# Kernel optimization log

Hardware: AMD Instinct MI355X
Metric: run time of the kernel (lower is better)

The kernel has to match this reference:

```python
import jax, jax.numpy as jnp
import numpy as np

B, S, HID, NH = 2, 2048, 1024, 16
HD = HID // NH  # head_dim = 64


def setup_inputs() -> dict:
    key = jax.random.key(0)
    ks = jax.random.split(key, 11)
    sc = 1.0 / np.sqrt(HID)
    inp = {
        "query": jax.random.normal(ks[0], (B, S, HID), jnp.float32),
        "key_": jax.random.normal(ks[1], (B, S, HID), jnp.float32),
        "value": jax.random.normal(ks[2], (B, S, HID), jnp.float32),
        "Wq": jax.random.normal(ks[3], (HID, HID), jnp.float32) * sc,
        "bq": jnp.zeros((HID,), jnp.float32),
        "Wk": jax.random.normal(ks[4], (HID, HID), jnp.float32) * sc,
        "bk": jnp.zeros((HID,), jnp.float32),
        "Wv": jax.random.normal(ks[5], (HID, HID), jnp.float32) * sc,
        "bv": jnp.zeros((HID,), jnp.float32),
        "Wo": jax.random.normal(ks[6], (HID, HID), jnp.float32) * sc,
        "bo": jnp.zeros((HID,), jnp.float32),
    }
    return inp


def _split_heads(x):
    # [B, S, HID] -> [B, NH, S, HD]
    return x.reshape(B, S, NH, HD).transpose(0, 2, 1, 3)


def reference(query, key_, value, Wq, bq, Wk, bk, Wv, bv, Wo, bo):
    q = _split_heads(query @ Wq + bq)
    k = _split_heads(key_ @ Wk + bk)
    v = _split_heads(value @ Wv + bv)
    scale = 1.0 / jnp.sqrt(jnp.asarray(HD, q.dtype))
    # [B, NH, S, S] scores (unfused attention, as in the original module)
    scores = jnp.einsum("bhqd,bhkd->bhqk", q, k) * scale
    attn = jax.nn.softmax(scores, axis=-1)
    ctx = jnp.einsum("bhqk,bhkd->bhqd", attn, v)  # [B, NH, S, HD]
    ctx = ctx.transpose(0, 2, 1, 3).reshape(B, S, HID)
    return ctx @ Wo + bo
```

## Files before the change

### kernel.cpp

```cpp
#include <hip/hip_runtime.h>


typedef unsigned short u16;
typedef unsigned int u32;
typedef __bf16 bf16x8 __attribute__((ext_vector_type(8)));
typedef float f32x4 __attribute__((ext_vector_type(4)));
typedef u16 u16x4 __attribute__((ext_vector_type(4)));

__device__ __forceinline__ u16 f2bf(float f) {
  __bf16 h = (__bf16)f;
  return *(u16*)&h;
}

__device__ __forceinline__ void gll16(const void* g, void* l) {
  __builtin_amdgcn_global_load_lds(
      (const __attribute__((address_space(1))) u32*)g,
      (__attribute__((address_space(3))) u32*)l, 16, 0, 0);
}

__global__ __launch_bounds__(256) void prep_kernel(
    const float* __restrict__ q32, const float* __restrict__ k32,
    const float* __restrict__ v32,
    u16* __restrict__ qb, u16* __restrict__ kb, u16* __restrict__ vb,
    const float* __restrict__ W0, const float* __restrict__ W1,
    const float* __restrict__ W2, const float* __restrict__ W3,
    u16* __restrict__ T0, u16* __restrict__ T1,
    u16* __restrict__ T2, u16* __restrict__ T3) {
  int blk = blockIdx.x, tid = threadIdx.x;
  if (blk < 12288) {
    int which = blk >> 12;
    const float* in = (which == 0) ? q32 : (which == 1) ? k32 : v32;
    u16* out = (which == 0) ? qb : (which == 1) ? kb : vb;
    int i = (blk & 4095) * 256 + tid;
    float4 v = ((const float4*)in)[i];
    u16x4 o;
    o.x = f2bf(v.x); o.y = f2bf(v.y); o.z = f2bf(v.z); o.w = f2bf(v.w);
    ((u16x4*)out)[i] = o;
  } else {
    int tb = blk - 12288;
    int z = tb >> 10, rest = tb & 1023;
    const float* W = (z == 0) ? W0 : (z == 1) ? W1 : (z == 2) ? W2 : W3;
    u16* WT = (z == 0) ? T0 : (z == 1) ? T1 : (z == 2) ? T2 : T3;
    __shared__ float t[32][33];
    int bx = (rest & 31) * 32, by = (rest >> 5) * 32;
    int tx = tid & 31, ty = tid >> 5;
#pragma unroll
    for (int i = ty; i < 32; i += 8) t[i][tx] = W[(by + i) * 1024 + bx + tx];
    __syncthreads();
#pragma unroll
    for (int i = ty; i < 32; i += 8) WT[(bx + i) * 1024 + by + tx] = f2bf(t[tx][i]);
  }
}

struct GemmJob {
  const u16* A; const u16* BT; const float* bias;
  float* Cf; u16* Cb; int mode; float oscale;
};

template <int BN>
__global__ __launch_bounds__(256, 4) void gemm_sbuf(GemmJob j0, GemmJob j1, GemmJob j2) {
  constexpr int NT = BN / 32;
  constexpr int NBC = BN / 32;
  const int K = 1024, N = 1024;
  __shared__ __align__(16) u16 As[128 * 64];
  __shared__ __align__(16) u16 Bs[BN * 64];
  int blk = blockIdx.x, tid = threadIdx.x;
  int z, r0, bm, bn;
  if (BN == 128) {
    z = blk >> 8; r0 = blk & 255;
    int xcd = r0 & 7, i5 = r0 >> 3;
    bm = (xcd * 4 + (i5 & 3)) * 128;
    bn = (i5 >> 2) * 128;
  } else {
    z = 0; r0 = blk;
    int xcd = r0 & 7, i6 = r0 >> 3;
    bm = (xcd * 4 + (i6 & 3)) * 128;
    bn = (i6 >> 2) * 64;
  }
  GemmJob j = (z == 0) ? j0 : (z == 1) ? j1 : j2;
  int w = tid >> 6, lane = tid & 63, quad = lane >> 4, l16 = lane & 15;
  int wr = (w >> 1) * 64, wc = (w & 1) * (BN / 2);
  f32x4 acc[4][NT] = {};

  auto stage = [&](int kk) {
#pragma unroll
    for (int i = 0; i < 4; ++i) {
      int c = tid + i * 256;
      int r = c >> 3, jp = c & 7, jg = jp ^ (r & 7);
      gll16(&j.A[(size_t)(bm + r) * K + kk + jg * 8], &As[c * 8]);
    }
#pragma unroll
    for (int i = 0; i < NBC; ++i) {
      int c = tid + i * 256;
      int r = c >> 3, jp = c & 7, jg = jp ^ (r & 7);
      gll16(&j.BT[(size_t)(bn + r) * K + kk + jg * 8], &Bs[c * 8]);
    }
  };

  for (int it = 0; it < 16; ++it) {
    __syncthreads();
    stage(it * 64);
    __syncthreads();
#pragma unroll
    for (int ks = 0; ks < 2; ++ks) {
      bf16x8 af[4], bfr[NT];
#pragma unroll
      for (int mt = 0; mt < 4; ++mt) {
        int row = wr + mt * 16 + l16;
        af[mt] = *(const bf16x8*)&As[row * 64 + (((ks * 4 + quad) ^ (row & 7))) * 8];
      }
#pragma unroll
      for (int nt = 0; nt < NT; ++nt) {
        int row = wc + nt * 16 + l16;
        bfr[nt] = *(const bf16x8*)&Bs[row * 64 + (((ks * 4 + quad) ^ (row & 7))) * 8];
      }
#pragma unroll
      for (int mt = 0; mt < 4; ++mt)
#pragma unroll
        for (int nt = 0; nt < NT; ++nt)
          acc[mt][nt] = __builtin_amdgcn_mfma_f32_16x16x32_bf16(af[mt], bfr[nt], acc[mt][nt], 0, 0, 0);
    }
  }

#pragma unroll
  for (int mt = 0; mt < 4; ++mt)
#pragma unroll
    for (int nt = 0; nt < NT; ++nt)
#pragma unroll
      for (int r = 0; r < 4; ++r) {
        int row = bm + wr + mt * 16 + quad * 4 + r;
        int col = bn + wc + nt * 16 + l16;
        float v = (acc[mt][nt][r] + j.bias[col]) * j.oscale;
        if (j.mode == 0) {
          j.Cf[(size_t)row * N + col] = v;
        } else {
          int b = row >> 11, s = row & 2047, h = col >> 6, d = col & 63;
          u16 bv = f2bf(v);
          if (j.mode == 1)
            j.Cb[(((size_t)(b * 16 + h) * 2048 + s) << 6) + d] = bv;
          else
            j.Cb[((size_t)(b * 16 + h) * 64 + d) * 2048 + s] = bv;
        }
      }
}

__global__ __launch_bounds__(512) void attn_kernel(
    const u16* __restrict__ Q,
    const u16* __restrict__ Kk,
    const u16* __restrict__ VT,
    u16* __restrict__ ctx)
{
  __shared__ __align__(16) u16 Ks[2][128 * 64];
  __shared__ __align__(16) u16 Vs[2][64 * 128];
  __shared__ __align__(16) u16 PT[8 * 16 * 32];

  int blk = blockIdx.x;
  int qt = (blk >> 3) & 15;
  int bh = (blk & 7) * 4 + (blk >> 7);
  int b = bh >> 4, h = bh & 15;
  const u16* Qb = Q + ((size_t)bh * 2048 + qt * 128) * 64;
  const u16* Kb = Kk + (size_t)bh * 2048 * 64;
  const u16* Vb = VT + (size_t)bh * 64 * 2048;
  int tid = threadIdx.x, w = tid >> 6, lane = tid & 63, quad = lane >> 4, l16 = lane & 15;
  int rowbase = w * 16;
  u16* PTw = &PT[w * 16 * 32];

  bf16x8 qf[2];
#pragma unroll
  for (int ks = 0; ks < 2; ++ks)
    qf[ks] = *(const bf16x8*)&Qb[(rowbase + l16) * 64 + ks * 32 + quad * 8];

  f32x4 Oacc[4] = {};
  float lacc = 0.f;

  auto stage = [&](int t, int sel) {
    int kbase = t * 128;
#pragma unroll
    for (int i = 0; i < 2; ++i) {
      int c = tid + i * 512;
      int r = c >> 3, jp = c & 7, jg = jp ^ (r & 7);
      gll16(&Kb[(size_t)(kbase + r) * 64 + jg * 8], &Ks[sel][c * 8]);
    }
#pragma unroll
    for (int i = 0; i < 2; ++i) {
      int c = tid + i * 512;
      int d = c >> 4, jp = c & 15, jg = jp ^ (d & 15);
      gll16(&Vb[(size_t)d * 2048 + kbase + jg * 8], &Vs[sel][c * 8]);
    }
  };

  stage(0, 0);
  __syncthreads();

  for (int kv = 0; kv < 16; ++kv) {
    int cur = kv & 1;
    if (kv < 15) stage(kv + 1, cur ^ 1);

#pragma unroll
    for (int c = 0; c < 4; ++c) {
      f32x4 Sc[2] = {};
      __builtin_amdgcn_s_setprio(1);
#pragma unroll
      for (int nt2 = 0; nt2 < 2; ++nt2) {
        int r = (c * 2 + nt2) * 16 + l16;
#pragma unroll
        for (int ks = 0; ks < 2; ++ks) {
          bf16x8 kfr = *(const bf16x8*)&Ks[cur][r * 64 + ((ks * 4 + quad) ^ (l16 & 7)) * 8];
          Sc[nt2] = __builtin_amdgcn_mfma_f32_16x16x32_bf16(kfr, qf[ks], Sc[nt2], 0, 0, 0);
        }
      }
      __builtin_amdgcn_s_setprio(0);

#pragma unroll
      for (int nt2 = 0; nt2 < 2; ++nt2) {
        u16x4 pk;
#pragma unroll
        for (int r = 0; r < 4; ++r) {
          float p = exp2f(Sc[nt2][r]);
          lacc += p;
          pk[r] = f2bf(p);
        }
        int jl = nt2 * 2 + (quad >> 1);
        *(u16x4*)&PTw[l16 * 32 + ((jl ^ (l16 & 3)) * 8) + (quad & 1) * 4] = pk;
      }

      bf16x8 pfB = *(const bf16x8*)&PTw[l16 * 32 + ((quad ^ (l16 & 3)) * 8)];
      __builtin_amdgcn_s_setprio(1);
#pragma unroll
      for (int dt = 0; dt < 4; ++dt) {
        int d = dt * 16 + l16;
        bf16x8 vf = *(const bf16x8*)&Vs[cur][d * 128 + (((c * 4 + quad) ^ l16)) * 8];
        Oacc[dt] = __builtin_amdgcn_mfma_f32_16x16x32_bf16(vf, pfB, Oacc[dt], 0, 0, 0);
      }
      __builtin_amdgcn_s_setprio(0);
    }

    __syncthreads();
  }

  float l = lacc;
  l += __shfl_xor(l, 16, 64);
  l += __shfl_xor(l, 32, 64);
  float linv = 1.0f / l;

  int s = qt * 128 + rowbase + l16;
#pragma unroll
  for (int dt = 0; dt < 4; ++dt) {
    u16x4 o;
#pragma unroll
    for (int r = 0; r < 4; ++r) o[r] = f2bf(Oacc[dt][r] * linv);
    *(u16x4*)&ctx[(size_t)(b * 2048 + s) * 1024 + h * 64 + dt * 16 + quad * 4] = o;
  }
}


extern "C" void kernel_launch(void* const* d_in, const int* in_sizes, int n_in,
                              void* d_out, int out_size, void* d_ws, size_t ws_size,
                              hipStream_t stream) {
  const float* query = (const float*)d_in[0];
  const float* key_  = (const float*)d_in[1];
  const float* value = (const float*)d_in[2];
  const float* Wq = (const float*)d_in[3];
  const float* bq = (const float*)d_in[4];
  const float* Wk = (const float*)d_in[5];
  const float* bk = (const float*)d_in[6];
  const float* Wv = (const float*)d_in[7];
  const float* bv = (const float*)d_in[8];
  const float* Wo = (const float*)d_in[9];
  const float* bo = (const float*)d_in[10];
  float* out = (float*)d_out;

  char* ws = (char*)d_ws;
  const size_t MB = 1024 * 1024;
  u16* Aq  = (u16*)(ws + 0 * MB);
  u16* Ak  = (u16*)(ws + 8 * MB);
  u16* Av  = (u16*)(ws + 16 * MB);
  u16* WqT = (u16*)(ws + 24 * MB);
  u16* WkT = (u16*)(ws + 26 * MB);
  u16* WvT = (u16*)(ws + 28 * MB);
  u16* WoT = (u16*)(ws + 30 * MB);
  u16* Qp  = (u16*)(ws + 32 * MB);
  u16* Kp  = (u16*)(ws + 40 * MB);
  u16* VTp = (u16*)(ws + 48 * MB);
  u16* Ctx = (u16*)(ws + 56 * MB);

  prep_kernel<<<16384, 256, 0, stream>>>(query, key_, value, Aq, Ak, Av,
                                         Wq, Wk, Wv, Wo, WqT, WkT, WvT, WoT);

  const float sc = 0.125f * 1.44269504f;
  GemmJob jq{Aq, WqT, bq, nullptr, Qp, 1, sc};
  GemmJob jk{Ak, WkT, bk, nullptr, Kp, 1, 1.0f};
  GemmJob jv{Av, WvT, bv, nullptr, VTp, 2, 1.0f};
  gemm_sbuf<128><<<768, 256, 0, stream>>>(jq, jk, jv);

  attn_kernel<<<512, 512, 0, stream>>>(Qp, Kp, VTp, Ctx);

  GemmJob jo{Ctx, WoT, bo, out, nullptr, 0, 1.0f};
  gemm_sbuf<64><<<512, 256, 0, stream>>>(jo, jo, jo);
}
```

Baseline: 245.8 us.

## Give each attention wave two 16-row query fragments, halving block threads

The attention kernel now runs 4 waves of 32 query rows each instead of 8 waves of 16 rows. Each K and V fragment read from LDS feeds two MFMAs, which halves LDS read traffic per unit of compute. The P transpose buffer switches from an XOR swizzle to a padded row stride of 40. The cost is more registers per wave, fewer waves per block for hiding latency, and twice the staging loads per thread.

```diff
diff --git a/kernel.cpp b/kernel.cpp
--- a/kernel.cpp
+++ b/kernel.cpp
@@ -144,7 +144,7 @@
       }
 }
 
-__global__ __launch_bounds__(512) void attn_kernel(
+__global__ __launch_bounds__(256) void attn_kernel(
     const u16* __restrict__ Q,
     const u16* __restrict__ Kk,
     const u16* __restrict__ VT,
@@ -152,7 +152,7 @@
 {
   __shared__ __align__(16) u16 Ks[2][128 * 64];
   __shared__ __align__(16) u16 Vs[2][64 * 128];
-  __shared__ __align__(16) u16 PT[8 * 16 * 32];
+  __shared__ __align__(16) u16 PT[4 * 32 * 40];
 
   int blk = blockIdx.x;
   int qt = (blk >> 3) & 15;
@@ -162,28 +162,30 @@
   const u16* Kb = Kk + (size_t)bh * 2048 * 64;
   const u16* Vb = VT + (size_t)bh * 64 * 2048;
   int tid = threadIdx.x, w = tid >> 6, lane = tid & 63, quad = lane >> 4, l16 = lane & 15;
-  int rowbase = w * 16;
-  u16* PTw = &PT[w * 16 * 32];
-
-  bf16x8 qf[2];
-#pragma unroll
-  for (int ks = 0; ks < 2; ++ks)
-    qf[ks] = *(const bf16x8*)&Qb[(rowbase + l16) * 64 + ks * 32 + quad * 8];
-
-  f32x4 Oacc[4] = {};
-  float lacc = 0.f;
+  int rowbase = w * 32;
+  u16* PTw = &PT[w * 32 * 40];
+
+  bf16x8 qf[2][2];
+#pragma unroll
+  for (int f = 0; f < 2; ++f)
+#pragma unroll
+    for (int ks = 0; ks < 2; ++ks)
+      qf[f][ks] = *(const bf16x8*)&Qb[(rowbase + f * 16 + l16) * 64 + ks * 32 + quad * 8];
+
+  f32x4 Oacc[2][4] = {};
+  float lacc0 = 0.f, lacc1 = 0.f;
 
   auto stage = [&](int t, int sel) {
     int kbase = t * 128;
 #pragma unroll
-    for (int i = 0; i < 2; ++i) {
-      int c = tid + i * 512;
+    for (int i = 0; i < 4; ++i) {
+      int c = tid + i * 256;
       int r = c >> 3, jp = c & 7, jg = jp ^ (r & 7);
       gll16(&Kb[(size_t)(kbase + r) * 64 + jg * 8], &Ks[sel][c * 8]);
     }
 #pragma unroll
-    for (int i = 0; i < 2; ++i) {
-      int c = tid + i * 512;
+    for (int i = 0; i < 4; ++i) {
+      int c = tid + i * 256;
       int d = c >> 4, jp = c & 15, jg = jp ^ (d & 15);
       gll16(&Vb[(size_t)d * 2048 + kbase + jg * 8], &Vs[sel][c * 8]);
     }
@@ -198,7 +200,7 @@
 
 #pragma unroll
     for (int c = 0; c < 4; ++c) {
-      f32x4 Sc[2] = {};
+      f32x4 Sc[2][2] = {};
       __builtin_amdgcn_s_setprio(1);
 #pragma unroll
       for (int nt2 = 0; nt2 < 2; ++nt2) {
@@ -206,31 +208,36 @@
 #pragma unroll
         for (int ks = 0; ks < 2; ++ks) {
           bf16x8 kfr = *(const bf16x8*)&Ks[cur][r * 64 + ((ks * 4 + quad) ^ (l16 & 7)) * 8];
-          Sc[nt2] = __builtin_amdgcn_mfma_f32_16x16x32_bf16(kfr, qf[ks], Sc[nt2], 0, 0, 0);
+          Sc[0][nt2] = __builtin_amdgcn_mfma_f32_16x16x32_bf16(kfr, qf[0][ks], Sc[0][nt2], 0, 0, 0);
+          Sc[1][nt2] = __builtin_amdgcn_mfma_f32_16x16x32_bf16(kfr, qf[1][ks], Sc[1][nt2], 0, 0, 0);
         }
       }
       __builtin_amdgcn_s_setprio(0);
 
 #pragma unroll
-      for (int nt2 = 0; nt2 < 2; ++nt2) {
-        u16x4 pk;
-#pragma unroll
-        for (int r = 0; r < 4; ++r) {
-          float p = exp2f(Sc[nt2][r]);
-          lacc += p;
-          pk[r] = f2bf(p);
+      for (int f = 0; f < 2; ++f)
+#pragma unroll
+        for (int nt2 = 0; nt2 < 2; ++nt2) {
+          u16x4 pk;
+#pragma unroll
+          for (int r = 0; r < 4; ++r) {
+            float p = exp2f(Sc[f][nt2][r]);
+            if (f == 0) lacc0 += p; else lacc1 += p;
+            pk[r] = f2bf(p);
+          }
+          int jl = nt2 * 2 + (quad >> 1);
+          *(u16x4*)&PTw[(f * 16 + l16) * 40 + jl * 8 + (quad & 1) * 4] = pk;
         }
-        int jl = nt2 * 2 + (quad >> 1);
-        *(u16x4*)&PTw[l16 * 32 + ((jl ^ (l16 & 3)) * 8) + (quad & 1) * 4] = pk;
-      }
-
-      bf16x8 pfB = *(const bf16x8*)&PTw[l16 * 32 + ((quad ^ (l16 & 3)) * 8)];
+
+      bf16x8 pfB0 = *(const bf16x8*)&PTw[(0 * 16 + l16) * 40 + quad * 8];
+      bf16x8 pfB1 = *(const bf16x8*)&PTw[(1 * 16 + l16) * 40 + quad * 8];
       __builtin_amdgcn_s_setprio(1);
 #pragma unroll
       for (int dt = 0; dt < 4; ++dt) {
         int d = dt * 16 + l16;
         bf16x8 vf = *(const bf16x8*)&Vs[cur][d * 128 + (((c * 4 + quad) ^ l16)) * 8];
-        Oacc[dt] = __builtin_amdgcn_mfma_f32_16x16x32_bf16(vf, pfB, Oacc[dt], 0, 0, 0);
+        Oacc[0][dt] = __builtin_amdgcn_mfma_f32_16x16x32_bf16(vf, pfB0, Oacc[0][dt], 0, 0, 0);
+        Oacc[1][dt] = __builtin_amdgcn_mfma_f32_16x16x32_bf16(vf, pfB1, Oacc[1][dt], 0, 0, 0);
       }
       __builtin_amdgcn_s_setprio(0);
     }
@@ -238,18 +245,20 @@
     __syncthreads();
   }
 
-  float l = lacc;
-  l += __shfl_xor(l, 16, 64);
-  l += __shfl_xor(l, 32, 64);
-  float linv = 1.0f / l;
-
-  int s = qt * 128 + rowbase + l16;
-#pragma unroll
-  for (int dt = 0; dt < 4; ++dt) {
-    u16x4 o;
-#pragma unroll
-    for (int r = 0; r < 4; ++r) o[r] = f2bf(Oacc[dt][r] * linv);
-    *(u16x4*)&ctx[(size_t)(b * 2048 + s) * 1024 + h * 64 + dt * 16 + quad * 4] = o;
+#pragma unroll
+  for (int f = 0; f < 2; ++f) {
+    float l = (f == 0) ? lacc0 : lacc1;
+    l += __shfl_xor(l, 16, 64);
+    l += __shfl_xor(l, 32, 64);
+    float linv = 1.0f / l;
+    int s = qt * 128 + rowbase + f * 16 + l16;
+#pragma unroll
+    for (int dt = 0; dt < 4; ++dt) {
+      u16x4 o;
+#pragma unroll
+      for (int r = 0; r < 4; ++r) o[r] = f2bf(Oacc[f][dt][r] * linv);
+      *(u16x4*)&ctx[(size_t)(b * 2048 + s) * 1024 + h * 64 + dt * 16 + quad * 4] = o;
+    }
   }
 }
 
@@ -293,7 +302,7 @@
   GemmJob jv{Av, WvT, bv, nullptr, VTp, 2, 1.0f};
   gemm_sbuf<128><<<768, 256, 0, stream>>>(jq, jk, jv);
 
-  attn_kernel<<<512, 512, 0, stream>>>(Qp, Kp, VTp, Ctx);
+  attn_kernel<<<512, 256, 0, stream>>>(Qp, Kp, VTp, Ctx);
 
   GemmJob jo{Ctx, WoT, bo, out, nullptr, 0, 1.0f};
   gemm_sbuf<64><<<512, 256, 0, stream>>>(jo, jo, jo);
```

New measurement: 238.2 us. 1.03x faster.
